# Kernel optimization log

Hardware: AMD Instinct MI355X
Metric: run time of the kernel (lower is better)

Reference implementation:

```python
import jax, jax.numpy as jnp
import numpy as np

B, T, D, U = 64, 512, 512, 1024


def setup_inputs() -> dict:
    key = jax.random.key(0)
    k1, k2, k3 = jax.random.split(key, 3)
    x = jax.random.normal(k1, (B, T, D), dtype=jnp.float32)
    kernel = jax.random.normal(k2, (D, 4 * U), dtype=jnp.float32) * (1.0 / np.sqrt(D))
    rec_kernel = jax.random.normal(k3, (U, 4 * U), dtype=jnp.float32) * (1.0 / np.sqrt(U))
    return {"x": x, "kernel": kernel, "rec_kernel": rec_kernel}


def reference(x, kernel, rec_kernel):
    """SimpleLSTM forward: returns last hidden state h_T of shape [B, U].
    Gate order along the 4U axis is (i, f, c, o), matching the kernel split.
    No biases; initial h and c are zeros (as in the original call()).
    """
    units = rec_kernel.shape[0]
    # Precompute input contributions for all timesteps in one big GEMM:
    # x_gates[b, t, :] == x[b, t] @ kernel  (same math as 4 per-gate matmuls)
    x_gates = jnp.einsum('btd,dk->tbk', x, kernel)  # [T, B, 4U]

    def step(carry, xt):
        h, c = carry
        z = xt + h @ rec_kernel  # [B, 4U]
        i = jax.nn.sigmoid(z[:, :units])
        f = jax.nn.sigmoid(z[:, units:2 * units])
        g = jnp.tanh(z[:, 2 * units:3 * units])
        o = jax.nn.sigmoid(z[:, 3 * units:])
        c_new = f * c + i * g
        h_new = o * jnp.tanh(c_new)
        return (h_new, c_new), None

    batch = x.shape[0]
    h0 = jnp.zeros((batch, units), dtype=x.dtype)
    c0 = jnp.zeros((batch, units), dtype=x.dtype)
    (h_last, _), _ = jax.lax.scan(step, (h0, c0), x_gates)
    return h_last
```

## Files before the change

### kernel.cpp

```cpp
#include <hip/hip_runtime.h>
#include <stdint.h>

#define WS_XB   0LL
#define WS_H    33554432LL
#define WS_FLAG 33816576LL

typedef unsigned short u16;
typedef unsigned int   u32;
typedef unsigned long long u64;
typedef __attribute__((ext_vector_type(8))) short short8;
typedef __attribute__((ext_vector_type(4))) float f32x4;

__device__ __forceinline__ u16 f2bf(float f) {
  unsigned u = __float_as_uint(f);
  u += 0x7FFFu + ((u >> 16) & 1u);
  return (u16)(u >> 16);
}
__device__ __forceinline__ float fast_tanh(float x) {
  float e = __expf(2.f * x);
  return 1.f - 2.f / (e + 1.f);
}

__global__ void conv_x(const float* __restrict__ x, u16* __restrict__ xb) {
  long gid = (long)blockIdx.x * blockDim.x + threadIdx.x;
  long sr = gid >> 6;
  int  d0 = (int)(gid & 63) * 8;
  int  b = (int)(sr >> 9), t = (int)(sr & 511);
  const float* src = x + sr * 512 + d0;
  float4 v0 = *(const float4*)(src);
  float4 v1 = *(const float4*)(src + 4);
  u16 tmp[8] = {f2bf(v0.x), f2bf(v0.y), f2bf(v0.z), f2bf(v0.w),
                f2bf(v1.x), f2bf(v1.y), f2bf(v1.z), f2bf(v1.w)};
  *(short8*)(xb + ((long)t * 64 + b) * 512 + d0) = *(short8*)tmp;
}

__launch_bounds__(256, 1)
__global__ void lstm_fused(const float* __restrict__ kern, const float* __restrict__ rec,
                           const u16* __restrict__ xb, u32* __restrict__ hbuf,
                           u32* __restrict__ flags, float* __restrict__ out) {
  __shared__ u16   smH[2][32 * 64 * 8];
  __shared__ float zscr[4][16][20];

  const int bid = blockIdx.x;
  const int bg = bid >> 6;
  const int ut = bid & 63;
  const int tid = threadIdx.x;
  const int w = tid >> 6, lane = tid & 63;
  const int quad = lane >> 4, n15 = lane & 15;
  const int gate = n15 >> 2, uu = n15 & 3;
  const int rowE = quad * 4 + gate;

  short8 wf[48];
  const size_t gcol = (size_t)gate * 1024 + (size_t)ut * 16 + (size_t)(w * 4 + uu);
#pragma unroll
  for (int ks = 0; ks < 32; ++ks) {
    u16 tmp[8];
#pragma unroll
    for (int j = 0; j < 8; ++j)
      tmp[j] = f2bf(rec[(size_t)(ks * 32 + quad * 8 + j) * 4096 + gcol]);
    wf[ks] = *(short8*)tmp;
  }
#pragma unroll
  for (int ks = 0; ks < 16; ++ks) {
    u16 tmp[8];
#pragma unroll
    for (int j = 0; j < 8; ++j)
      tmp[j] = f2bf(kern[(size_t)(ks * 32 + quad * 8 + j) * 4096 + gcol]);
    wf[32 + ks] = *(short8*)tmp;
  }

  float c = 0.f;

#pragma unroll
  for (int j = 0; j < 8; ++j)
    *(uint4*)(&smH[0][(tid + j * 256) * 8]) = (uint4){0u, 0u, 0u, 0u};

  short8 xf[16];
  {
    const u16* xr = xb + (size_t)(bg * 16 + n15) * 512 + quad * 8;
#pragma unroll
    for (int ks = 0; ks < 16; ++ks) xf[ks] = *(const short8*)(xr + ks * 32);
  }
  f32x4 acc0 = {0.f, 0.f, 0.f, 0.f}, acc1 = {0.f, 0.f, 0.f, 0.f};
#pragma unroll
  for (int ks = 0; ks < 16; ks += 2) {
    acc0 = __builtin_amdgcn_mfma_f32_16x16x32_bf16(xf[ks], wf[32 + ks], acc0, 0, 0, 0);
    acc1 = __builtin_amdgcn_mfma_f32_16x16x32_bf16(xf[ks + 1], wf[33 + ks], acc1, 0, 0, 0);
  }
  __syncthreads();

#define X16_MFMA                                                                   \
  _Pragma("unroll")                                                                \
  for (int ks2 = 0; ks2 < 16; ks2 += 2) {                                          \
    acc0 = __builtin_amdgcn_mfma_f32_16x16x32_bf16(xf[ks2], wf[32 + ks2], acc0, 0, 0, 0);     \
    acc1 = __builtin_amdgcn_mfma_f32_16x16x32_bf16(xf[ks2 + 1], wf[33 + ks2], acc1, 0, 0, 0); \
  }

#define PAYLOAD_LOAD                                                               \
  {                                                                                \
    const u32* hs = hbuf + (size_t)pb * 32768 + (size_t)(bg * 16 + n15) * 512 + quad * 4; \
    _Pragma("unroll")                                                              \
    for (int kk = 0; kk < 8; ++kk) {                                               \
      const u64* src = (const u64*)(hs + (w * 8 + kk) * 16);                       \
      pay[2 * kk]     = __hip_atomic_load(src,     __ATOMIC_RELAXED, __HIP_MEMORY_SCOPE_AGENT); \
      pay[2 * kk + 1] = __hip_atomic_load(src + 1, __ATOMIC_RELAXED, __HIP_MEMORY_SCOPE_AGENT); \
    }                                                                              \
  }

#define OWN8(BASE)                                                                 \
  _Pragma("unroll")                                                                \
  for (int kk = 0; kk < 8; ++kk) {                                                 \
    union { u64 q[2]; short8 s; u32 d[4]; } uo;                                    \
    uo.q[0] = pay[2 * kk]; uo.q[1] = pay[2 * kk + 1];                              \
    if (kk & 1) acc1 = __builtin_amdgcn_mfma_f32_16x16x32_bf16(uo.s, wf[(BASE) + kk], acc1, 0, 0, 0); \
    else        acc0 = __builtin_amdgcn_mfma_f32_16x16x32_bf16(uo.s, wf[(BASE) + kk], acc0, 0, 0, 0); \
    *(uint4*)(smH[pb] + (((BASE) + kk) * 64 + lane) * 8) =                         \
        (uint4){uo.d[0], uo.d[1], uo.d[2], uo.d[3]};                               \
  }

  for (int t = 0; t < 512; ++t) {
    const u16* sh = smH[t & 1];
#pragma unroll
    for (int g = 0; g < 4; ++g) {
      if (g == w) continue;
#pragma unroll
      for (int kk = 0; kk < 8; kk += 2) {
        const int ks = g * 8 + kk;
        short8 a0 = *(const short8*)(sh + (ks * 64 + lane) * 8);
        acc0 = __builtin_amdgcn_mfma_f32_16x16x32_bf16(a0, wf[ks], acc0, 0, 0, 0);
        short8 a1 = *(const short8*)(sh + ((ks + 1) * 64 + lane) * 8);
        acc1 = __builtin_amdgcn_mfma_f32_16x16x32_bf16(a1, wf[ks + 1], acc1, 0, 0, 0);
      }
    }

    const int cw = uu * 4 + gate;
    zscr[w][quad * 4 + 0][cw] = acc0[0] + acc1[0];
    zscr[w][quad * 4 + 1][cw] = acc0[1] + acc1[1];
    zscr[w][quad * 4 + 2][cw] = acc0[2] + acc1[2];
    zscr[w][quad * 4 + 3][cw] = acc0[3] + acc1[3];
    asm volatile("s_waitcnt lgkmcnt(0)" ::: "memory");
    __builtin_amdgcn_sched_barrier(0);
    float4 zv = *(const float4*)&zscr[w][rowE][uu * 4];

    float ig = 1.f / (1.f + __expf(-zv.x));
    float fg = 1.f / (1.f + __expf(-zv.y));
    float gg = fast_tanh(zv.z);
    float og = 1.f / (1.f + __expf(-zv.w));
    c = fg * c + ig * gg;
    float h = og * fast_tanh(c);

    if (t == 511) {
      out[(size_t)(bg * 16 + rowE) * 1024 + (size_t)(ut * 16 + w * 4 + uu)] = h;
      break;
    }

    const int pb = (t + 1) & 1;

    {
      u16 hu = f2bf(h);
      int other = __shfl_xor((int)(unsigned)hu, 1);
      if ((uu & 1) == 0) {
        u32 pw = (u32)hu | ((u32)(unsigned)other << 16);
        __hip_atomic_store(&hbuf[(size_t)pb * 32768 + (size_t)(bg * 16 + rowE) * 512
                                 + ut * 8 + w * 2 + (uu >> 1)],
                           pw, __ATOMIC_RELAXED, __HIP_MEMORY_SCOPE_AGENT);
      }
    }

    {
      const u16* xr = xb + ((size_t)(t + 1) * 64 + bg * 16 + n15) * 512 + quad * 8;
#pragma unroll
      for (int ks2 = 0; ks2 < 16; ++ks2) xf[ks2] = *(const short8*)(xr + ks2 * 32);
    }

    asm volatile("s_waitcnt vmcnt(0)" ::: "memory");
    asm volatile("s_barrier" ::: "memory");
    if (tid == 0)
      __hip_atomic_store(&flags[(bg * 64 + ut) * 32], (u32)(t + 1),
                         __ATOMIC_RELAXED, __HIP_MEMORY_SCOPE_AGENT);

    acc0 = (f32x4){0.f, 0.f, 0.f, 0.f};
    acc1 = (f32x4){0.f, 0.f, 0.f, 0.f};

    u64 pay[16];
    if (w == 0) {
      const u32 tgt = (u32)(t + 1);
      const u32* fp = &flags[(bg * 64 + lane) * 32];
      u32 v = __hip_atomic_load(fp, __ATOMIC_RELAXED, __HIP_MEMORY_SCOPE_AGENT);
      while (__ballot(v < tgt) != 0ull) {
        __builtin_amdgcn_s_sleep(1);
        v = __hip_atomic_load(fp, __ATOMIC_RELAXED, __HIP_MEMORY_SCOPE_AGENT);
      }
      PAYLOAD_LOAD;
    } else {
      X16_MFMA;
    }
    asm volatile("s_barrier" ::: "memory");
    if (w == 0) {
      X16_MFMA;
    } else {
      PAYLOAD_LOAD;
    }

    if      (w == 0) { OWN8(0)  }
    else if (w == 1) { OWN8(8)  }
    else if (w == 2) { OWN8(16) }
    else             { OWN8(24) }

    asm volatile("s_waitcnt lgkmcnt(0)" ::: "memory");
    asm volatile("s_barrier" ::: "memory");
  }
}

extern "C" void kernel_launch(void* const* d_in, const int* in_sizes, int n_in,
                              void* d_out, int out_size, void* d_ws, size_t ws_size,
                              hipStream_t stream) {
  const float* x    = (const float*)d_in[0];
  const float* kern = (const float*)d_in[1];
  const float* rec  = (const float*)d_in[2];
  float* out = (float*)d_out;
  char* ws = (char*)d_ws;

  u16* xbp   = (u16*)(ws + WS_XB);
  u32* hbuf  = (u32*)(ws + WS_H);
  u32* flags = (u32*)(ws + WS_FLAG);

  hipMemsetAsync(ws + WS_FLAG, 0, 32768, stream);

  conv_x<<<8192, 256, 0, stream>>>(x, xbp);

  lstm_fused<<<256, 256, 0, stream>>>(kern, rec, xbp, hbuf, flags, out);
}
```

Baseline: 3.351 ms.

## Use per-wave flags and drop block barrier in LSTM step handoff

Each wave now publishes its own flag after storing its slice of h, so the block-wide barrier before the flag store is gone. Every wave polls the producer flags for the 16 rows it needs and then loads its payload itself, replacing the scheme where wave 0 polled alone and the others waited at a barrier. The x-projection MFMAs now run before the flag store, and the x tile for step t+2 is prefetched one step ahead, so the wait on that load leaves the critical path. This cuts synchronisation latency in the recurrent loop. In exchange there is four times as much flag polling traffic across all waves, and the pipelined xf register buffer must stay correct at the last step.

```diff
diff --git a/kernel.cpp b/kernel.cpp
--- a/kernel.cpp
+++ b/kernel.cpp
@@ -87,6 +87,11 @@
     acc0 = __builtin_amdgcn_mfma_f32_16x16x32_bf16(xf[ks], wf[32 + ks], acc0, 0, 0, 0);
     acc1 = __builtin_amdgcn_mfma_f32_16x16x32_bf16(xf[ks + 1], wf[33 + ks], acc1, 0, 0, 0);
   }
+  {
+    const u16* xr = xb + ((size_t)1 * 64 + bg * 16 + n15) * 512 + quad * 8;
+#pragma unroll
+    for (int ks = 0; ks < 16; ++ks) xf[ks] = *(const short8*)(xr + ks * 32);
+  }
   __syncthreads();
 
 #define X16_MFMA                                                                   \
@@ -155,6 +160,7 @@
     }
 
     const int pb = (t + 1) & 1;
+    const u32 tag = (u32)(t + 1);
 
     {
       u16 hu = f2bf(h);
@@ -167,41 +173,37 @@
       }
     }
 
-    {
-      const u16* xr = xb + ((size_t)(t + 1) * 64 + bg * 16 + n15) * 512 + quad * 8;
-#pragma unroll
-      for (int ks2 = 0; ks2 < 16; ++ks2) xf[ks2] = *(const short8*)(xr + ks2 * 32);
-    }
-
-    asm volatile("s_waitcnt vmcnt(0)" ::: "memory");
-    asm volatile("s_barrier" ::: "memory");
-    if (tid == 0)
-      __hip_atomic_store(&flags[(bg * 64 + ut) * 32], (u32)(t + 1),
-                         __ATOMIC_RELAXED, __HIP_MEMORY_SCOPE_AGENT);
-
     acc0 = (f32x4){0.f, 0.f, 0.f, 0.f};
     acc1 = (f32x4){0.f, 0.f, 0.f, 0.f};
+    X16_MFMA;
+
+    asm volatile("s_waitcnt vmcnt(0)" ::: "memory");
+    if (lane == 0)
+      __hip_atomic_store(&flags[(bg * 64 + ut) * 32 + w], tag,
+                         __ATOMIC_RELAXED, __HIP_MEMORY_SCOPE_AGENT);
+
+    {
+      const int tn = (t + 2 < 512) ? (t + 2) : 511;
+      const u16* xr = xb + ((size_t)tn * 64 + bg * 16 + n15) * 512 + quad * 8;
+#pragma unroll
+      for (int ks2 = 0; ks2 < 16; ++ks2) xf[ks2] = *(const short8*)(xr + ks2 * 32);
+    }
+
+    {
+      const u32* fp = &flags[(bg * 64 + w * 16 + (lane & 15)) * 32];
+      for (;;) {
+        u32 f0 = __hip_atomic_load(fp + 0, __ATOMIC_RELAXED, __HIP_MEMORY_SCOPE_AGENT);
+        u32 f1 = __hip_atomic_load(fp + 1, __ATOMIC_RELAXED, __HIP_MEMORY_SCOPE_AGENT);
+        u32 f2 = __hip_atomic_load(fp + 2, __ATOMIC_RELAXED, __HIP_MEMORY_SCOPE_AGENT);
+        u32 f3 = __hip_atomic_load(fp + 3, __ATOMIC_RELAXED, __HIP_MEMORY_SCOPE_AGENT);
+        u32 mn = min(min(f0, f1), min(f2, f3));
+        if (__ballot(mn < tag) == 0ull) break;
+        __builtin_amdgcn_s_sleep(1);
+      }
+    }
 
     u64 pay[16];
-    if (w == 0) {
-      const u32 tgt = (u32)(t + 1);
-      const u32* fp = &flags[(bg * 64 + lane) * 32];
-      u32 v = __hip_atomic_load(fp, __ATOMIC_RELAXED, __HIP_MEMORY_SCOPE_AGENT);
-      while (__ballot(v < tgt) != 0ull) {
-        __builtin_amdgcn_s_sleep(1);
-        v = __hip_atomic_load(fp, __ATOMIC_RELAXED, __HIP_MEMORY_SCOPE_AGENT);
-      }
-      PAYLOAD_LOAD;
-    } else {
-      X16_MFMA;
-    }
-    asm volatile("s_barrier" ::: "memory");
-    if (w == 0) {
-      X16_MFMA;
-    } else {
-      PAYLOAD_LOAD;
-    }
-
+    PAYLOAD_LOAD;
     if      (w == 0) { OWN8(0)  }
     else if (w == 1) { OWN8(8)  }
     else if (w == 2) { OWN8(16) }
```

New measurement: 3.520 ms. 1.05x slower.
